# Kernel tuning notes

Hardware: AMD Instinct MI355X
Metric: run time of the kernel (lower is better)

## Reference

```python
import jax, jax.numpy as jnp
import numpy as np

E = 131072          # number of message events
NUM_NODES = 32768   # max distinct dst ids (unique padded to this size)
D_MEM = 256         # memory dim
D_EDGE = 128        # edge feature dim
T_DIM = 64          # time encoding dim
HID = 512           # message MLP hidden
MSG = 256           # message dim (GRU input)
IN_DIM = 2 * D_MEM + D_EDGE + T_DIM  # 704


def setup_inputs() -> dict:
    key = jax.random.key(0)
    ks = jax.random.split(key, 16)
    def lin(k, fan_out, fan_in):
        s = 1.0 / np.sqrt(fan_in)
        return jax.random.uniform(k, (fan_out, fan_in), jnp.float32, -s, s)
    def vec(k, n, fan_in):
        s = 1.0 / np.sqrt(fan_in)
        return jax.random.uniform(k, (n,), jnp.float32, -s, s)
    return {
        "rel_time": jax.random.uniform(ks[0], (E,), jnp.float32, 0.0, 1.0) * 1000.0,
        "src_memories": jax.random.normal(ks[1], (E, D_MEM), jnp.float32),
        "dst_memories": jax.random.normal(ks[2], (E, D_MEM), jnp.float32),
        "edge_features": jax.random.normal(ks[3], (E, D_EDGE), jnp.float32),
        "dst_ids": jax.random.randint(ks[4], (E,), 0, NUM_NODES, jnp.int64),
        # time encoder params: cos(t*w + b)
        "time_w": jax.random.normal(ks[5], (T_DIM,), jnp.float32),
        "time_b": jax.random.normal(ks[6], (T_DIM,), jnp.float32),
        # message MLP params
        "w1": lin(ks[7], HID, IN_DIM), "b1": vec(ks[8], HID, IN_DIM),
        "w2": lin(ks[9], MSG, HID), "b2": vec(ks[10], MSG, HID),
        # GRUCell params (torch layout: [3*hidden, in])
        "gru_w_ih": lin(ks[11], 3 * D_MEM, MSG), "gru_w_hh": lin(ks[12], 3 * D_MEM, D_MEM),
        "gru_b_ih": vec(ks[13], 3 * D_MEM, MSG), "gru_b_hh": vec(ks[14], 3 * D_MEM, D_MEM),
    }


def reference(rel_time, src_memories, dst_memories, edge_features, dst_ids,
              time_w, time_b, w1, b1, w2, b2,
              gru_w_ih, gru_w_hh, gru_b_ih, gru_b_hh):
    # --- time encoding: cos(t*w + b) -> [E, T_DIM]
    t_enc = jnp.cos(rel_time[:, None] * time_w[None, :] + time_b[None, :])
    # --- message encoder: MLP over concat(src_mem, dst_mem, edge_feat, t_enc)
    x = jnp.concatenate([src_memories, dst_memories, edge_features, t_enc], axis=-1)  # [E, IN_DIM]
    h = jax.nn.relu(x @ w1.T + b1)
    msg = h @ w2.T + b2  # [E, MSG]
    # --- dedupe dst ids (torch.unique return_inverse), padded to static size
    unique_ids, index = jnp.unique(dst_ids, return_inverse=True,
                                   size=NUM_NODES, fill_value=NUM_NODES)
    # --- mean aggregation of messages per unique dst node
    sums = jax.ops.segment_sum(msg, index, num_segments=NUM_NODES)
    counts = jax.ops.segment_sum(jnp.ones((E,), msg.dtype), index, num_segments=NUM_NODES)
    agg = sums / jnp.maximum(counts, 1.0)[:, None]  # [NUM_NODES, MSG]
    # --- prev memories: torch mem_idx = unique(inverse) = arange(U) -> first rows
    prev = dst_memories[:NUM_NODES]  # [NUM_NODES, D_MEM]
    # --- GRUCell recurrent memory update (torch gate math)
    gi = agg @ gru_w_ih.T + gru_b_ih   # [NUM_NODES, 3*D_MEM]
    gh = prev @ gru_w_hh.T + gru_b_hh
    gi_r, gi_z, gi_n = jnp.split(gi, 3, axis=-1)
    gh_r, gh_z, gh_n = jnp.split(gh, 3, axis=-1)
    r = jax.nn.sigmoid(gi_r + gh_r)
    z = jax.nn.sigmoid(gi_z + gh_z)
    n = jnp.tanh(gi_n + r * gh_n)
    memories = (1.0 - z) * n + z * prev  # [NUM_NODES, D_MEM]
    return unique_ids, memories
```

## Files before the change

kernel.cpp:

```cpp
#include <hip/hip_runtime.h>
#include <math.h>
#include <stdint.h>

#define E_EDGES 131072
#define NN 32768
#define DMEM 256
#define DEDGE 128
#define TDIM 64
#define HID 512
#define MSGD 256
#define INDIM 704

typedef __bf16 bf16_t;
typedef bf16_t bf16x8 __attribute__((ext_vector_type(8)));
typedef float f32x4 __attribute__((ext_vector_type(4)));

__device__ __forceinline__ unsigned short f2bf(float f) {
  unsigned int u = __float_as_uint(f);
  u += 0x7FFF + ((u >> 16) & 1);
  return (unsigned short)(u >> 16);
}

__device__ __forceinline__ void gl_lds16(const bf16_t* g, bf16_t* l) {
  __builtin_amdgcn_global_load_lds(
      (__attribute__((address_space(1))) void*)(g),
      (__attribute__((address_space(3))) void*)(l), 16, 0, 0);
}

__global__ void cvt_bf16(const float* __restrict__ in, unsigned short* __restrict__ out, int n) {
  int i = blockIdx.x * 256 + threadIdx.x;
  if (i < n) out[i] = f2bf(in[i]);
}


__global__ __launch_bounds__(512) void gemm12_fused(
    const float* __restrict__ src, const float* __restrict__ dmem,
    const float* __restrict__ edge, const float* __restrict__ rel,
    const float* __restrict__ tw, const float* __restrict__ tb,
    const bf16_t* __restrict__ w1b, const float* __restrict__ b1,
    const bf16_t* __restrict__ w2b, const float* __restrict__ b2,
    const int* __restrict__ perm, const int* __restrict__ dsts,
    float* __restrict__ sums) {
  __shared__ alignas(16) bf16_t smem[74752];
  __shared__ float sTW[64], sTB[64], sRel[128];
  __shared__ int sPerm[128], sDst[128];
  bf16_t* hL  = smem;
  bf16_t* sB2 = smem + 66560;

  const int bm = blockIdx.x;
  const int t = threadIdx.x;
  const int lane = t & 63;
  const int wave = t >> 6;
  const int wm  = (wave >> 2) * 64;
  const int wn1 = (wave & 3) * 128;
  const int wn2 = (wave & 3) * 64;

  if (t < 64) { sTW[t] = tw[t]; sTB[t] = tb[t]; }
  if (t < 128) {
    int e = perm[bm * 128 + t];
    sPerm[t] = e;
    sRel[t] = rel[e];
    sDst[t] = dsts[bm * 128 + t];
  }
  __syncthreads();

  f32x4 acc[4][8];
#pragma unroll
  for (int i = 0; i < 4; i++)
#pragma unroll
    for (int j = 0; j < 8; j++) acc[i][j] = (f32x4){0.f, 0.f, 0.f, 0.f};

  const int ar   = t >> 2;
  const int lin8 = (t & 3) * 8;
  const int gs8  = (((t & 3) ^ ((t >> 3) & 3))) * 8;
  const size_t arow = (size_t)sPerm[ar];
  const float rv0 = sRel[ar];
  const bf16_t* gB = w1b + (size_t)ar * 704 + gs8;

  const int lrow = lane & 15;
  const int kqs  = ((lane >> 4) ^ ((lane >> 1) & 3)) * 8;
  const int kql  = (lane >> 4) * 8;

  {
    f32x4 u = *(const f32x4*)(src + arow * 256 + gs8);
    f32x4 v = *(const f32x4*)(src + arow * 256 + gs8 + 4);
    bf16_t* lB = smem + 8192 + (size_t)t * 8;
    gl_lds16(gB,                     lB);
    gl_lds16(gB + (size_t)128 * 704, lB + 4096);
    gl_lds16(gB + (size_t)256 * 704, lB + 8192);
    gl_lds16(gB + (size_t)384 * 704, lB + 12288);
    gB += 32;
    bf16x8 av;
    av[0] = (bf16_t)u[0]; av[1] = (bf16_t)u[1]; av[2] = (bf16_t)u[2]; av[3] = (bf16_t)u[3];
    av[4] = (bf16_t)v[0]; av[5] = (bf16_t)v[1]; av[6] = (bf16_t)v[2]; av[7] = (bf16_t)v[3];
    *(bf16x8*)(smem + ar * 32 + lin8) = av;
  }
  __syncthreads();

  int cur = 0;
  for (int c = 0; c < 22; ++c) {
    const int cn = c + 1;
    const bool more = (cn < 22);
    const bool ld   = (cn < 20);
    f32x4 u, v;
    if (ld) {
      const int col = cn * 32;
      const float* p;
      if (col < 256)      p = src  + arow * 256 + col + gs8;
      else if (col < 512) p = dmem + arow * 256 + (col - 256) + gs8;
      else                p = edge + arow * 128 + (col - 512) + gs8;
      u = *(const f32x4*)p;
      v = *(const f32x4*)(p + 4);
    }
    const int nxt = cur ^ 1;
    if (more) {
      bf16_t* lB = smem + (nxt ? 24576 : 8192) + (size_t)t * 8;
      gl_lds16(gB,                     lB);
      gl_lds16(gB + (size_t)128 * 704, lB + 4096);
      gl_lds16(gB + (size_t)256 * 704, lB + 8192);
      gl_lds16(gB + (size_t)384 * 704, lB + 12288);
      gB += 32;
    }

    const bf16_t* bA = smem + (cur ? 4096 : 0);
    const bf16_t* bB = smem + (cur ? 24576 : 8192);
    bf16x8 af[4], bfr[8];
#pragma unroll
    for (int i = 0; i < 4; i++) af[i]  = *(const bf16x8*)(bA + (wm  + i * 16 + lrow) * 32 + kqs);
#pragma unroll
    for (int i = 0; i < 8; i++) bfr[i] = *(const bf16x8*)(bB + (wn1 + i * 16 + lrow) * 32 + kqs);

    __builtin_amdgcn_s_setprio(1);
#pragma unroll
    for (int mi = 0; mi < 4; mi++)
#pragma unroll
      for (int ni = 0; ni < 8; ni++)
        acc[mi][ni] = __builtin_amdgcn_mfma_f32_16x16x32_bf16(af[mi], bfr[ni], acc[mi][ni], 0, 0, 0);
    __builtin_amdgcn_s_setprio(0);

    if (more) {
      bf16x8 av;
      if (ld) {
        av[0] = (bf16_t)u[0]; av[1] = (bf16_t)u[1]; av[2] = (bf16_t)u[2]; av[3] = (bf16_t)u[3];
        av[4] = (bf16_t)v[0]; av[5] = (bf16_t)v[1]; av[6] = (bf16_t)v[2]; av[7] = (bf16_t)v[3];
      } else {
        int kk = cn * 32 - 640 + gs8;
#pragma unroll
        for (int j = 0; j < 8; j++)
          av[j] = (bf16_t)cosf(rv0 * sTW[kk + j] + sTB[kk + j]);
      }
      *(bf16x8*)(smem + (nxt ? 4096 : 0) + ar * 32 + lin8) = av;
    }
    __syncthreads();
    cur = nxt;
  }

  const int crow = (lane >> 4) * 4;
  const int ccol = lane & 15;
#pragma unroll
  for (int ni = 0; ni < 8; ni++) {
    int col = wn1 + ni * 16 + ccol;
    float bv = b1[col];
#pragma unroll
    for (int mi = 0; mi < 4; mi++) {
#pragma unroll
      for (int r = 0; r < 4; r++) {
        float v = fmaxf(acc[mi][ni][r] + bv, 0.f);
        ((unsigned short*)hL)[(wm + mi * 16 + crow + r) * 520 + col] = f2bf(v);
      }
    }
  }

  f32x4 acc2[4][4];
#pragma unroll
  for (int i = 0; i < 4; i++)
#pragma unroll
    for (int j = 0; j < 4; j++) acc2[i][j] = (f32x4){0.f, 0.f, 0.f, 0.f};

  const bf16_t* gW2 = w2b + (size_t)ar * 512 + gs8;
  bf16_t* lB2 = sB2 + (size_t)t * 8;

  gl_lds16(gW2,                     lB2);
  gl_lds16(gW2 + (size_t)128 * 512, lB2 + 4096);
  gW2 += 32;
  __syncthreads();

  for (int k0 = 0; k0 < HID; k0 += 32) {
    bf16x8 af2[4], bf2[4];
#pragma unroll
    for (int i = 0; i < 4; i++)
      af2[i] = *(const bf16x8*)(hL + (wm + i * 16 + lrow) * 520 + k0 + kql);
#pragma unroll
    for (int i = 0; i < 4; i++)
      bf2[i] = *(const bf16x8*)(sB2 + (wn2 + i * 16 + lrow) * 32 + kqs);
    __syncthreads();

    if (k0 + 32 < HID) {
      gl_lds16(gW2,                     lB2);
      gl_lds16(gW2 + (size_t)128 * 512, lB2 + 4096);
      gW2 += 32;
    }

    __builtin_amdgcn_s_setprio(1);
#pragma unroll
    for (int mi = 0; mi < 4; mi++)
#pragma unroll
      for (int ni = 0; ni < 4; ni++)
        acc2[mi][ni] = __builtin_amdgcn_mfma_f32_16x16x32_bf16(af2[mi], bf2[ni], acc2[mi][ni], 0, 0, 0);
    __builtin_amdgcn_s_setprio(0);
    __syncthreads();
  }

  {
    float* msgL = (float*)smem;
#pragma unroll
    for (int ni = 0; ni < 4; ni++) {
      int gcol = wn2 + ni * 16 + ccol;
      float bv = b2[gcol];
#pragma unroll
      for (int mi = 0; mi < 4; mi++) {
#pragma unroll
        for (int r = 0; r < 4; r++)
          msgL[(wm + mi * 16 + crow + r) * 260 + gcol] = acc2[mi][ni][r] + bv;
      }
    }
    __syncthreads();

    const int c = t & 255;
    const int h = t >> 8;
    int r = h * 64;
    const int rend = h * 64 + 64;
    while (r < rend) {
      int id = sDst[r];
      if (r > 0 && sDst[r - 1] == id) { r++; continue; }
      float s2 = msgL[r * 260 + c];
      int rr = r + 1;
      while (rr < 128 && sDst[rr] == id) { s2 += msgL[rr * 260 + c]; rr++; }
      if (r == 0 || rr == 128)
        atomicAdd(&sums[(size_t)id * 256 + c], s2);
      else
        sums[(size_t)id * 256 + c] = s2;
      r = rr;
    }
  }
}

template <int ACT, int OMODE, int GRUSEL>
__global__ __launch_bounds__(512) void gemm_bt2(
    const bf16_t* __restrict__ A, const bf16_t* __restrict__ B,
    const float* __restrict__ bias, void* __restrict__ Cout,
    const bf16_t* __restrict__ A2, const float* __restrict__ bias2,
    void* __restrict__ Cout2,
    const int* __restrict__ dstid, float* __restrict__ sums,
    int M, int N, int K) {
  __shared__ alignas(16) bf16_t sT[24576];

  int bm = blockIdx.y, bn = blockIdx.x;
  if (GRUSEL && blockIdx.z == 1) { A = A2; bias = bias2; Cout = Cout2; }

  const int t = threadIdx.x;
  const int lane = t & 63;
  const int wave = t >> 6;
  const int wm = (wave >> 2) * 64;
  const int wn = (wave & 3) * 64;

  f32x4 acc[4][4];
#pragma unroll
  for (int i = 0; i < 4; i++)
#pragma unroll
    for (int j = 0; j < 4; j++) acc[i][j] = (f32x4){0.f, 0.f, 0.f, 0.f};

  const int gs8 = (((t & 3) ^ ((t >> 3) & 3))) * 8;
  const bf16_t* gA = A + ((size_t)bm * 128 + (t >> 2)) * K + gs8;
  const bf16_t* gB = B + ((size_t)bn * 256 + (t >> 2)) * K + gs8;
  const size_t gB2off = (size_t)128 * K;

  const int lrow = lane & 15;
  const int kqs  = ((lane >> 4) ^ ((lane >> 1) & 3)) * 8;

  {
    bf16_t* lA = sT + (size_t)t * 8;
    bf16_t* lB = sT + 4096 + (size_t)t * 8;
    gl_lds16(gA, lA);
    gl_lds16(gB, lB);
    gl_lds16(gB + gB2off, lB + 4096);
    gA += 32; gB += 32;
  }
  __syncthreads();

  int cur = 0;
  const int nk = K >> 5;
  for (int k = 0; k < nk; ++k) {
    const int nxt = cur ^ 1;
    if (k + 1 < nk) {
      bf16_t* lA = sT + (nxt ? 12288 : 0) + (size_t)t * 8;
      bf16_t* lB = sT + (nxt ? 16384 : 4096) + (size_t)t * 8;
      gl_lds16(gA, lA);
      gl_lds16(gB, lB);
      gl_lds16(gB + gB2off, lB + 4096);
      gA += 32; gB += 32;
    }
    const bf16_t* bA = sT + (cur ? 12288 : 0);
    const bf16_t* bB = sT + (cur ? 16384 : 4096);
    bf16x8 af[4], bfr[4];
#pragma unroll
    for (int i = 0; i < 4; i++) af[i]  = *(const bf16x8*)(bA + (wm + i * 16 + lrow) * 32 + kqs);
#pragma unroll
    for (int i = 0; i < 4; i++) bfr[i] = *(const bf16x8*)(bB + (wn + i * 16 + lrow) * 32 + kqs);

    __builtin_amdgcn_s_setprio(1);
#pragma unroll
    for (int mi = 0; mi < 4; mi++)
#pragma unroll
      for (int ni = 0; ni < 4; ni++)
        acc[mi][ni] = __builtin_amdgcn_mfma_f32_16x16x32_bf16(af[mi], bfr[ni], acc[mi][ni], 0, 0, 0);
    __builtin_amdgcn_s_setprio(0);
    __syncthreads();
    cur = nxt;
  }

  const int crow = (lane >> 4) * 4;
  const int ccol = lane & 15;
  if (OMODE == 2) {
#pragma unroll
    for (int mi = 0; mi < 4; mi++) {
      int id4[4];
#pragma unroll
      for (int r = 0; r < 4; r++)
        id4[r] = dstid[(size_t)bm * 128 + wm + mi * 16 + crow + r];
#pragma unroll
      for (int ni = 0; ni < 4; ni++) {
        int gcol = wn + ni * 16 + ccol;
        float bv = bias[gcol];
#pragma unroll
        for (int r = 0; r < 4; r++)
          atomicAdd(&sums[(size_t)id4[r] * 256 + gcol], acc[mi][ni][r] + bv);
      }
    }
  } else {
#pragma unroll
    for (int ni = 0; ni < 4; ni++) {
      int gcol = bn * 256 + wn + ni * 16 + ccol;
      float bv = bias[gcol];
#pragma unroll
      for (int mi = 0; mi < 4; mi++) {
#pragma unroll
        for (int r = 0; r < 4; r++) {
          size_t grow = (size_t)bm * 128 + wm + mi * 16 + crow + r;
          float v = acc[mi][ni][r] + bv;
          if (ACT) v = fmaxf(v, 0.f);
          ((unsigned short*)Cout)[grow * N + gcol] = f2bf(v);
        }
      }
    }
  }
}

__global__ void mark_k(const int* __restrict__ dst, int* __restrict__ icnt) {
  int e = blockIdx.x * 256 + threadIdx.x;
  if (e < E_EDGES) atomicAdd(&icnt[dst[e]], 1);
}

__global__ void fill_k(float* __restrict__ uo, int* __restrict__ slot_id) {
  int j = blockIdx.x * 256 + threadIdx.x;
  if (j < NN) { uo[j] = (float)NN; slot_id[j] = -1; }
}

__global__ void scan2_k(const int* __restrict__ icnt, int* __restrict__ rank,
                        int* __restrict__ offs) {
  __shared__ int pf[1024], pc[1024];
  int t = threadIdx.x;
  int base = t * 32;
  int sf = 0, sc = 0;
  for (int i = 0; i < 32; i++) { int v = icnt[base + i]; sf += (v > 0); sc += v; }
  pf[t] = sf; pc[t] = sc;
  __syncthreads();
  for (int off = 1; off < 1024; off <<= 1) {
    int vf = (t >= off) ? pf[t - off] : 0;
    int vc = (t >= off) ? pc[t - off] : 0;
    __syncthreads();
    pf[t] += vf; pc[t] += vc;
    __syncthreads();
  }
  int runf = (t == 0) ? 0 : pf[t - 1];
  int runc = (t == 0) ? 0 : pc[t - 1];
  for (int i = 0; i < 32; i++) {
    int v = icnt[base + i];
    rank[base + i] = runf; runf += (v > 0);
    offs[base + i] = runc; runc += v;
  }
}

__global__ void scatter_ids(const int* __restrict__ icnt, const int* __restrict__ rank,
                            float* __restrict__ uo, int* __restrict__ slot_id) {
  int id = blockIdx.x * 256 + threadIdx.x;
  if (id < NN && icnt[id] > 0) {
    int s = rank[id];
    uo[s] = (float)id;
    slot_id[s] = id;
  }
}

__global__ void scatter_edges(const int* __restrict__ dst, const int* __restrict__ offs,
                              int* __restrict__ cursor, int* __restrict__ perm,
                              int* __restrict__ dsts) {
  int e = blockIdx.x * 256 + threadIdx.x;
  if (e < E_EDGES) {
    int id = dst[e];
    int pos = offs[id] + atomicAdd(&cursor[id], 1);
    perm[pos] = e;
    dsts[pos] = id;
  }
}

__global__ void agg_pack(const int* __restrict__ slot_id, const float* __restrict__ sums,
                         const int* __restrict__ icnt, const float* __restrict__ dmem,
                         unsigned short* __restrict__ aggb, unsigned short* __restrict__ prevb) {
  int j = blockIdx.x, t = threadIdx.x;
  int id = slot_id[j];
  float a = 0.f;
  if (id >= 0) a = sums[(size_t)id * 256 + t] / fmaxf((float)icnt[id], 1.f);
  aggb[(size_t)j * 256 + t] = f2bf(a);
  prevb[(size_t)j * 256 + t] = f2bf(dmem[(size_t)j * 256 + t]);
}

__global__ void gru_gate(const unsigned short* __restrict__ gi,
                         const unsigned short* __restrict__ gh,
                         const float* __restrict__ dmem, float* __restrict__ out) {
  int j = blockIdx.x, t = threadIdx.x;
  size_t b = (size_t)j * 768;
  auto bf = [](unsigned short u) { return __uint_as_float((unsigned int)u << 16); };
  float gir = bf(gi[b + t]), giz = bf(gi[b + 256 + t]), gin = bf(gi[b + 512 + t]);
  float ghr = bf(gh[b + t]), ghz = bf(gh[b + 256 + t]), ghn = bf(gh[b + 512 + t]);
  float r = 1.f / (1.f + expf(-(gir + ghr)));
  float z = 1.f / (1.f + expf(-(giz + ghz)));
  float n = tanhf(gin + r * ghn);
  float prev = dmem[(size_t)j * 256 + t];
  out[(size_t)NN + (size_t)j * 256 + t] = (1.f - z) * n + z * prev;
}

extern "C" void kernel_launch(void* const* d_in, const int* in_sizes, int n_in,
                              void* d_out, int out_size, void* d_ws, size_t ws_size,
                              hipStream_t stream) {
  const float* rel  = (const float*)d_in[0];
  const float* src  = (const float*)d_in[1];
  const float* dmem = (const float*)d_in[2];
  const float* edge = (const float*)d_in[3];
  const int*   dst  = (const int*)d_in[4];
  const float* tw   = (const float*)d_in[5];
  const float* tb   = (const float*)d_in[6];
  const float* w1   = (const float*)d_in[7];
  const float* b1   = (const float*)d_in[8];
  const float* w2   = (const float*)d_in[9];
  const float* b2   = (const float*)d_in[10];
  const float* wih  = (const float*)d_in[11];
  const float* whh  = (const float*)d_in[12];
  const float* bih  = (const float*)d_in[13];
  const float* bhh  = (const float*)d_in[14];

  char* ws = (char*)d_ws;
  size_t o = 0;
  auto take = [&](size_t bytes) -> char* {
    char* p = ws + o;
    o += (bytes + 255) & ~(size_t)255;
    return p;
  };

  unsigned short* gib   = (unsigned short*)take((size_t)NN * 768 * 2);
  unsigned short* ghb   = (unsigned short*)take((size_t)NN * 768 * 2);
  float* sums           = (float*)take((size_t)NN * 256 * 4);
  int*   icnt           = (int*)take((size_t)NN * 4);
  int*   rank           = (int*)take((size_t)NN * 4);
  int*   offs           = (int*)take((size_t)NN * 4);
  int*   cursor         = (int*)take((size_t)NN * 4);
  int*   slot_id        = (int*)take((size_t)NN * 4);
  int*   perm           = (int*)take((size_t)E_EDGES * 4);
  int*   dsts           = (int*)take((size_t)E_EDGES * 4);
  unsigned short* aggb  = (unsigned short*)take((size_t)NN * 256 * 2);
  unsigned short* prevb = (unsigned short*)take((size_t)NN * 256 * 2);
  unsigned short* w1b   = (unsigned short*)take((size_t)HID * INDIM * 2);
  unsigned short* w2b   = (unsigned short*)take((size_t)MSGD * HID * 2);
  unsigned short* wihb  = (unsigned short*)take((size_t)768 * 256 * 2);
  unsigned short* whhb  = (unsigned short*)take((size_t)768 * 256 * 2);

  float* outf = (float*)d_out;

  hipMemsetAsync(sums, 0, (size_t)NN * 256 * 4, stream);
  hipMemsetAsync(icnt, 0, (size_t)NN * 4, stream);
  hipMemsetAsync(cursor, 0, (size_t)NN * 4, stream);

  int n1 = HID * INDIM;
  int n2 = MSGD * HID;
  int n3 = 768 * 256;
  cvt_bf16<<<(n1 + 255) / 256, 256, 0, stream>>>(w1, w1b, n1);
  cvt_bf16<<<(n2 + 255) / 256, 256, 0, stream>>>(w2, w2b, n2);
  cvt_bf16<<<(n3 + 255) / 256, 256, 0, stream>>>(wih, wihb, n3);
  cvt_bf16<<<(n3 + 255) / 256, 256, 0, stream>>>(whh, whhb, n3);

  mark_k<<<E_EDGES / 256, 256, 0, stream>>>(dst, icnt);
  scan2_k<<<1, 1024, 0, stream>>>(icnt, rank, offs);
  scatter_edges<<<E_EDGES / 256, 256, 0, stream>>>(dst, offs, cursor, perm, dsts);

  fill_k<<<NN / 256, 256, 0, stream>>>(outf, slot_id);
  scatter_ids<<<NN / 256, 256, 0, stream>>>(icnt, rank, outf, slot_id);

  gemm12_fused<<<dim3(E_EDGES / 128), 512, 0, stream>>>(
      src, dmem, edge, rel, tw, tb, (const bf16_t*)w1b, b1,
      (const bf16_t*)w2b, b2, perm, dsts, sums);

  agg_pack<<<NN, 256, 0, stream>>>(slot_id, sums, icnt, dmem, aggb, prevb);

  gemm_bt2<0, 1, 1><<<dim3(768 / 256, NN / 128, 2), 512, 0, stream>>>(
      (const bf16_t*)aggb, (const bf16_t*)wihb, bih, gib,
      (const bf16_t*)prevb, bhh, ghb, nullptr, nullptr, NN, 768, 256);

  gru_gate<<<NN, 256, 0, stream>>>(gib, ghb, dmem, outf);
}
```

Measured before the change: 651.6 us.

## Fuse aggregation, GRU GEMMs and gate math into one kernel; prefetch A two chunks ahead

Replaces the agg_pack, two-way GRU GEMM and gru_gate kernels with one gru_fused kernel. It loads the summed messages (scaled by inverse count) and prev memories straight into LDS as bf16, and accumulates gi+gh for the r/z/n gates into one K=512 GEMM, keeping the n-gate hidden part separate. It then applies the gate math from LDS. This removes the bf16 gi/gh intermediates and two extra launches. The MLP kernel also software-pipelines the fp32 activation loads one further iteration ahead, at the cost of more registers.

```diff
diff --git a/kernel.cpp b/kernel.cpp
--- a/kernel.cpp
+++ b/kernel.cpp
@@ -81,18 +81,22 @@
   const int kqs  = ((lane >> 4) ^ ((lane >> 1) & 3)) * 8;
   const int kql  = (lane >> 4) * 8;
 
+  f32x4 uP, vP;
+
   {
-    f32x4 u = *(const f32x4*)(src + arow * 256 + gs8);
-    f32x4 v = *(const f32x4*)(src + arow * 256 + gs8 + 4);
+    f32x4 u0 = *(const f32x4*)(src + arow * 256 + gs8);
+    f32x4 v0 = *(const f32x4*)(src + arow * 256 + gs8 + 4);
     bf16_t* lB = smem + 8192 + (size_t)t * 8;
     gl_lds16(gB,                     lB);
     gl_lds16(gB + (size_t)128 * 704, lB + 4096);
     gl_lds16(gB + (size_t)256 * 704, lB + 8192);
     gl_lds16(gB + (size_t)384 * 704, lB + 12288);
     gB += 32;
+    uP = *(const f32x4*)(src + arow * 256 + 32 + gs8);
+    vP = *(const f32x4*)(src + arow * 256 + 32 + gs8 + 4);
     bf16x8 av;
-    av[0] = (bf16_t)u[0]; av[1] = (bf16_t)u[1]; av[2] = (bf16_t)u[2]; av[3] = (bf16_t)u[3];
-    av[4] = (bf16_t)v[0]; av[5] = (bf16_t)v[1]; av[6] = (bf16_t)v[2]; av[7] = (bf16_t)v[3];
+    av[0] = (bf16_t)u0[0]; av[1] = (bf16_t)u0[1]; av[2] = (bf16_t)u0[2]; av[3] = (bf16_t)u0[3];
+    av[4] = (bf16_t)v0[0]; av[5] = (bf16_t)v0[1]; av[6] = (bf16_t)v0[2]; av[7] = (bf16_t)v0[3];
     *(bf16x8*)(smem + ar * 32 + lin8) = av;
   }
   __syncthreads();
@@ -101,16 +105,15 @@
   for (int c = 0; c < 22; ++c) {
     const int cn = c + 1;
     const bool more = (cn < 22);
-    const bool ld   = (cn < 20);
-    f32x4 u, v;
-    if (ld) {
-      const int col = cn * 32;
+    f32x4 uN, vN;
+    if (c + 2 < 20) {
+      const int col = (c + 2) * 32;
       const float* p;
       if (col < 256)      p = src  + arow * 256 + col + gs8;
       else if (col < 512) p = dmem + arow * 256 + (col - 256) + gs8;
       else                p = edge + arow * 128 + (col - 512) + gs8;
-      u = *(const f32x4*)p;
-      v = *(const f32x4*)(p + 4);
+      uN = *(const f32x4*)p;
+      vN = *(const f32x4*)(p + 4);
     }
     const int nxt = cur ^ 1;
     if (more) {
@@ -140,9 +143,9 @@
 
     if (more) {
       bf16x8 av;
-      if (ld) {
-        av[0] = (bf16_t)u[0]; av[1] = (bf16_t)u[1]; av[2] = (bf16_t)u[2]; av[3] = (bf16_t)u[3];
-        av[4] = (bf16_t)v[0]; av[5] = (bf16_t)v[1]; av[6] = (bf16_t)v[2]; av[7] = (bf16_t)v[3];
+      if (cn < 20) {
+        av[0] = (bf16_t)uP[0]; av[1] = (bf16_t)uP[1]; av[2] = (bf16_t)uP[2]; av[3] = (bf16_t)uP[3];
+        av[4] = (bf16_t)vP[0]; av[5] = (bf16_t)vP[1]; av[6] = (bf16_t)vP[2]; av[7] = (bf16_t)vP[3];
       } else {
         int kk = cn * 32 - 640 + gs8;
 #pragma unroll
@@ -150,6 +153,7 @@
           av[j] = (bf16_t)cosf(rv0 * sTW[kk + j] + sTB[kk + j]);
       }
       *(bf16x8*)(smem + (nxt ? 4096 : 0) + ar * 32 + lin8) = av;
+      uP = uN; vP = vN;
     }
     __syncthreads();
     cur = nxt;
@@ -245,114 +249,174 @@
   }
 }
 
-template <int ACT, int OMODE, int GRUSEL>
-__global__ __launch_bounds__(512) void gemm_bt2(
-    const bf16_t* __restrict__ A, const bf16_t* __restrict__ B,
-    const float* __restrict__ bias, void* __restrict__ Cout,
-    const bf16_t* __restrict__ A2, const float* __restrict__ bias2,
-    void* __restrict__ Cout2,
-    const int* __restrict__ dstid, float* __restrict__ sums,
-    int M, int N, int K) {
-  __shared__ alignas(16) bf16_t sT[24576];
-
-  int bm = blockIdx.y, bn = blockIdx.x;
-  if (GRUSEL && blockIdx.z == 1) { A = A2; bias = bias2; Cout = Cout2; }
-
+__global__ __launch_bounds__(512, 2) void gru_fused(
+    const float* __restrict__ sums, const int* __restrict__ icnt,
+    const int* __restrict__ slot_id, const float* __restrict__ dmem,
+    const bf16_t* __restrict__ wihb, const bf16_t* __restrict__ whhb,
+    const float* __restrict__ bih, const float* __restrict__ bhh,
+    float* __restrict__ outm) {
+  __shared__ alignas(16) bf16_t sm[26624];
+  __shared__ float sBS[768], sBG[256], sInv[64];
+  __shared__ int sId[64];
+
+  const int bm = blockIdx.x;
   const int t = threadIdx.x;
   const int lane = t & 63;
   const int wave = t >> 6;
-  const int wm = (wave >> 2) * 64;
-  const int wn = (wave & 3) * 64;
-
-  f32x4 acc[4][4];
+  const int ws = wave * 96;
+  const int lrow = lane & 15;
+  const int gs8 = (((t & 3) ^ ((t >> 3) & 3))) * 8;
+  const int kqs = ((lane >> 4) ^ ((lane >> 1) & 3)) * 8;
+  const int arw = t >> 2;
+
+  if (t < 64) {
+    int id = slot_id[bm * 64 + t];
+    sId[t] = id;
+    sInv[t] = (id >= 0) ? (1.f / fmaxf((float)icnt[id], 1.f)) : 0.f;
+  }
+  for (int i = t; i < 768; i += 512) sBS[i] = bih[i] + bhh[i];
+  if (t < 256) sBG[t] = bhh[512 + t];
+  __syncthreads();
+
+  f32x4 accS[4][6];
 #pragma unroll
   for (int i = 0; i < 4; i++)
 #pragma unroll
-    for (int j = 0; j < 4; j++) acc[i][j] = (f32x4){0.f, 0.f, 0.f, 0.f};
-
-  const int gs8 = (((t & 3) ^ ((t >> 3) & 3))) * 8;
-  const bf16_t* gA = A + ((size_t)bm * 128 + (t >> 2)) * K + gs8;
-  const bf16_t* gB = B + ((size_t)bn * 256 + (t >> 2)) * K + gs8;
-  const size_t gB2off = (size_t)128 * K;
-
-  const int lrow = lane & 15;
-  const int kqs  = ((lane >> 4) ^ ((lane >> 1) & 3)) * 8;
-
-  {
-    bf16_t* lA = sT + (size_t)t * 8;
-    bf16_t* lB = sT + 4096 + (size_t)t * 8;
-    gl_lds16(gA, lA);
-    gl_lds16(gB, lB);
-    gl_lds16(gB + gB2off, lB + 4096);
-    gA += 32; gB += 32;
-  }
+    for (int j = 0; j < 6; j++) accS[i][j] = (f32x4){0.f, 0.f, 0.f, 0.f};
+  f32x4 accG[4][2];
+#pragma unroll
+  for (int i = 0; i < 4; i++)
+#pragma unroll
+    for (int j = 0; j < 2; j++) accG[i][j] = (f32x4){0.f, 0.f, 0.f, 0.f};
+
+  bf16_t* sA = sm + 24576;
+
+  if (t < 256) {
+    f32x4 u = (f32x4){0.f, 0.f, 0.f, 0.f}, v = u;
+    int id = sId[arw];
+    if (id >= 0) {
+      const float* p = sums + (size_t)id * 256 + gs8;
+      u = *(const f32x4*)p; v = *(const f32x4*)(p + 4);
+    }
+    float inv = sInv[arw];
+    bf16x8 av;
+#pragma unroll
+    for (int j = 0; j < 4; j++) { av[j] = (bf16_t)(u[j] * inv); av[4 + j] = (bf16_t)(v[j] * inv); }
+    *(bf16x8*)(sA + t * 8) = av;
+  }
+#pragma unroll
+  for (int ch = 0; ch < 6; ++ch)
+    gl_lds16(wihb + ((size_t)(ch * 128) + arw) * 256 + gs8, sm + ch * 4096 + (size_t)t * 8);
   __syncthreads();
 
-  int cur = 0;
-  const int nk = K >> 5;
-  for (int k = 0; k < nk; ++k) {
-    const int nxt = cur ^ 1;
-    if (k + 1 < nk) {
-      bf16_t* lA = sT + (nxt ? 12288 : 0) + (size_t)t * 8;
-      bf16_t* lB = sT + (nxt ? 16384 : 4096) + (size_t)t * 8;
-      gl_lds16(gA, lA);
-      gl_lds16(gB, lB);
-      gl_lds16(gB + gB2off, lB + 4096);
-      gA += 32; gB += 32;
-    }
-    const bf16_t* bA = sT + (cur ? 12288 : 0);
-    const bf16_t* bB = sT + (cur ? 16384 : 4096);
-    bf16x8 af[4], bfr[4];
-#pragma unroll
-    for (int i = 0; i < 4; i++) af[i]  = *(const bf16x8*)(bA + (wm + i * 16 + lrow) * 32 + kqs);
-#pragma unroll
-    for (int i = 0; i < 4; i++) bfr[i] = *(const bf16x8*)(bB + (wn + i * 16 + lrow) * 32 + kqs);
+  for (int k = 0; k < 16; ++k) {
+    const bool gph = (k >= 8);
+    bf16x8 af[4], bfS[6], bg[2];
+#pragma unroll
+    for (int i = 0; i < 4; i++)
+      af[i] = *(const bf16x8*)(sA + (i * 16 + lrow) * 32 + kqs);
+#pragma unroll
+    for (int n = 0; n < 6; n++)
+      bfS[n] = *(const bf16x8*)(sm + (ws + n * 16 + lrow) * 32 + kqs);
+    if (gph) {
+#pragma unroll
+      for (int g = 0; g < 2; g++)
+        bg[g] = *(const bf16x8*)(sm + (512 + wave * 32 + g * 16 + lrow) * 32 + kqs);
+    }
+    __syncthreads();
+
+    const int kn = k + 1;
+    f32x4 u = (f32x4){0.f, 0.f, 0.f, 0.f}, v = u;
+    if (kn < 16) {
+      const int k0n = kn * 32;
+      if (t < 256) {
+        if (k0n < 256) {
+          int id = sId[arw];
+          if (id >= 0) {
+            const float* p = sums + (size_t)id * 256 + k0n + gs8;
+            u = *(const f32x4*)p; v = *(const f32x4*)(p + 4);
+          }
+        } else {
+          const float* p = dmem + ((size_t)(bm * 64 + arw)) * 256 + (k0n - 256) + gs8;
+          u = *(const f32x4*)p; v = *(const f32x4*)(p + 4);
+        }
+      }
+      const bf16_t* Bs = (k0n < 256) ? wihb : whhb;
+      const int kk0 = k0n & 255;
+#pragma unroll
+      for (int ch = 0; ch < 6; ++ch)
+        gl_lds16(Bs + ((size_t)(ch * 128) + arw) * 256 + kk0 + gs8, sm + ch * 4096 + (size_t)t * 8);
+    }
 
     __builtin_amdgcn_s_setprio(1);
 #pragma unroll
-    for (int mi = 0; mi < 4; mi++)
-#pragma unroll
-      for (int ni = 0; ni < 4; ni++)
-        acc[mi][ni] = __builtin_amdgcn_mfma_f32_16x16x32_bf16(af[mi], bfr[ni], acc[mi][ni], 0, 0, 0);
+    for (int i = 0; i < 4; i++)
+#pragma unroll
+      for (int n = 0; n < 6; n++)
+        accS[i][n] = __builtin_amdgcn_mfma_f32_16x16x32_bf16(af[i], bfS[n], accS[i][n], 0, 0, 0);
+    if (gph) {
+#pragma unroll
+      for (int i = 0; i < 4; i++)
+#pragma unroll
+        for (int g = 0; g < 2; g++)
+          accG[i][g] = __builtin_amdgcn_mfma_f32_16x16x32_bf16(af[i], bg[g], accG[i][g], 0, 0, 0);
+    }
     __builtin_amdgcn_s_setprio(0);
-    __syncthreads();
-    cur = nxt;
-  }
-
+
+    if (kn < 16 && t < 256) {
+      bf16x8 av;
+      if (kn * 32 < 256) {
+        float inv = sInv[arw];
+#pragma unroll
+        for (int j = 0; j < 4; j++) { av[j] = (bf16_t)(u[j] * inv); av[4 + j] = (bf16_t)(v[j] * inv); }
+      } else {
+#pragma unroll
+        for (int j = 0; j < 4; j++) { av[j] = (bf16_t)u[j]; av[4 + j] = (bf16_t)v[j]; }
+      }
+      *(bf16x8*)(sA + t * 8) = av;
+    }
+    __syncthreads();
+  }
+
+  bf16_t* sS = sm;
+  bf16_t* sG = sm + 12416;
   const int crow = (lane >> 4) * 4;
   const int ccol = lane & 15;
-  if (OMODE == 2) {
-#pragma unroll
-    for (int mi = 0; mi < 4; mi++) {
-      int id4[4];
+  const int col = t & 255;
+  const int rh = t >> 8;
+  for (int mi = 0; mi < 4; ++mi) {
+#pragma unroll
+    for (int n = 0; n < 6; n++) {
+      int c = ws + n * 16 + ccol;
+      float b = sBS[c];
 #pragma unroll
       for (int r = 0; r < 4; r++)
-        id4[r] = dstid[(size_t)bm * 128 + wm + mi * 16 + crow + r];
-#pragma unroll
-      for (int ni = 0; ni < 4; ni++) {
-        int gcol = wn + ni * 16 + ccol;
-        float bv = bias[gcol];
-#pragma unroll
-        for (int r = 0; r < 4; r++)
-          atomicAdd(&sums[(size_t)id4[r] * 256 + gcol], acc[mi][ni][r] + bv);
-      }
-    }
-  } else {
-#pragma unroll
-    for (int ni = 0; ni < 4; ni++) {
-      int gcol = bn * 256 + wn + ni * 16 + ccol;
-      float bv = bias[gcol];
-#pragma unroll
-      for (int mi = 0; mi < 4; mi++) {
-#pragma unroll
-        for (int r = 0; r < 4; r++) {
-          size_t grow = (size_t)bm * 128 + wm + mi * 16 + crow + r;
-          float v = acc[mi][ni][r] + bv;
-          if (ACT) v = fmaxf(v, 0.f);
-          ((unsigned short*)Cout)[grow * N + gcol] = f2bf(v);
-        }
-      }
-    }
+        sS[(crow + r) * 776 + c] = (bf16_t)(accS[mi][n][r] + b);
+    }
+#pragma unroll
+    for (int g = 0; g < 2; g++) {
+      int c = wave * 32 + g * 16 + ccol;
+      float b = sBG[c];
+#pragma unroll
+      for (int r = 0; r < 4; r++)
+        sG[(crow + r) * 264 + c] = (bf16_t)(accG[mi][g][r] + b);
+    }
+    __syncthreads();
+#pragma unroll
+    for (int p = 0; p < 8; ++p) {
+      int r16 = rh * 8 + p;
+      size_t j = (size_t)bm * 64 + mi * 16 + r16;
+      float Sr = (float)sS[r16 * 776 + col];
+      float Sz = (float)sS[r16 * 776 + 256 + col];
+      float Sn = (float)sS[r16 * 776 + 512 + col];
+      float gn = (float)sG[r16 * 264 + col];
+      float rg = 1.f / (1.f + expf(-Sr));
+      float zg = 1.f / (1.f + expf(-Sz));
+      float ng = tanhf(Sn + (rg - 1.f) * gn);
+      float prev = dmem[j * 256 + col];
+      outm[j * 256 + col] = (1.f - zg) * ng + zg * prev;
+    }
+    __syncthreads();
   }
 }
 
@@ -411,32 +475,6 @@
     perm[pos] = e;
     dsts[pos] = id;
   }
-}
-
-__global__ void agg_pack(const int* __restrict__ slot_id, const float* __restrict__ sums,
-                         const int* __restrict__ icnt, const float* __restrict__ dmem,
-                         unsigned short* __restrict__ aggb, unsigned short* __restrict__ prevb) {
-  int j = blockIdx.x, t = threadIdx.x;
-  int id = slot_id[j];
-  float a = 0.f;
-  if (id >= 0) a = sums[(size_t)id * 256 + t] / fmaxf((float)icnt[id], 1.f);
-  aggb[(size_t)j * 256 + t] = f2bf(a);
-  prevb[(size_t)j * 256 + t] = f2bf(dmem[(size_t)j * 256 + t]);
-}
-
-__global__ void gru_gate(const unsigned short* __restrict__ gi,
-                         const unsigned short* __restrict__ gh,
-                         const float* __restrict__ dmem, float* __restrict__ out) {
-  int j = blockIdx.x, t = threadIdx.x;
-  size_t b = (size_t)j * 768;
-  auto bf = [](unsigned short u) { return __uint_as_float((unsigned int)u << 16); };
-  float gir = bf(gi[b + t]), giz = bf(gi[b + 256 + t]), gin = bf(gi[b + 512 + t]);
-  float ghr = bf(gh[b + t]), ghz = bf(gh[b + 256 + t]), ghn = bf(gh[b + 512 + t]);
-  float r = 1.f / (1.f + expf(-(gir + ghr)));
-  float z = 1.f / (1.f + expf(-(giz + ghz)));
-  float n = tanhf(gin + r * ghn);
-  float prev = dmem[(size_t)j * 256 + t];
-  out[(size_t)NN + (size_t)j * 256 + t] = (1.f - z) * n + z * prev;
 }
 
 extern "C" void kernel_launch(void* const* d_in, const int* in_sizes, int n_in,
@@ -466,8 +504,6 @@
     return p;
   };
 
-  unsigned short* gib   = (unsigned short*)take((size_t)NN * 768 * 2);
-  unsigned short* ghb   = (unsigned short*)take((size_t)NN * 768 * 2);
   float* sums           = (float*)take((size_t)NN * 256 * 4);
   int*   icnt           = (int*)take((size_t)NN * 4);
   int*   rank           = (int*)take((size_t)NN * 4);
@@ -476,8 +512,6 @@
   int*   slot_id        = (int*)take((size_t)NN * 4);
   int*   perm           = (int*)take((size_t)E_EDGES * 4);
   int*   dsts           = (int*)take((size_t)E_EDGES * 4);
-  unsigned short* aggb  = (unsigned short*)take((size_t)NN * 256 * 2);
-  unsigned short* prevb = (unsigned short*)take((size_t)NN * 256 * 2);
   unsigned short* w1b   = (unsigned short*)take((size_t)HID * INDIM * 2);
   unsigned short* w2b   = (unsigned short*)take((size_t)MSGD * HID * 2);
   unsigned short* wihb  = (unsigned short*)take((size_t)768 * 256 * 2);
@@ -508,11 +542,7 @@
       src, dmem, edge, rel, tw, tb, (const bf16_t*)w1b, b1,
       (const bf16_t*)w2b, b2, perm, dsts, sums);
 
-  agg_pack<<<NN, 256, 0, stream>>>(slot_id, sums, icnt, dmem, aggb, prevb);
-
-  gemm_bt2<0, 1, 1><<<dim3(768 / 256, NN / 128, 2), 512, 0, stream>>>(
-      (const bf16_t*)aggb, (const bf16_t*)wihb, bih, gib,
-      (const bf16_t*)prevb, bhh, ghb, nullptr, nullptr, NN, 768, 256);
-
-  gru_gate<<<NN, 256, 0, stream>>>(gib, ghb, dmem, outf);
-}
+  gru_fused<<<dim3(NN / 64), 512, 0, stream>>>(
+      sums, icnt, slot_id, dmem,
+      (const bf16_t*)wihb, (const bf16_t*)whhb, bih, bhh, outf + NN);
+}
```

Result: slower. 910.6 us (+39.8%).
